# Optimization experiments

Hardware: AMD Instinct MI355X
Metric: run time of the kernel (lower is better)

The kernel has to match this reference:

```python
import jax, jax.numpy as jnp
import numpy as np

EMB = 768
HEADS = 12
HEAD_DIM = EMB // HEADS
SEQ = 4096
BATCH = 1


def setup_inputs() -> dict:
    key = jax.random.key(0)
    ks = jax.random.split(key, 9)
    s = 1.0 / np.sqrt(EMB)
    return {
        "x": jax.random.normal(ks[0], (BATCH, SEQ, EMB), dtype=jnp.float32),
        "wq": jax.random.normal(ks[1], (EMB, EMB), dtype=jnp.float32) * s,
        "bq": jax.random.normal(ks[2], (EMB,), dtype=jnp.float32) * s,
        "wk": jax.random.normal(ks[3], (EMB, EMB), dtype=jnp.float32) * s,
        "bk": jax.random.normal(ks[4], (EMB,), dtype=jnp.float32) * s,
        "wv": jax.random.normal(ks[5], (EMB, EMB), dtype=jnp.float32) * s,
        "bv": jax.random.normal(ks[6], (EMB,), dtype=jnp.float32) * s,
        "wo": jax.random.normal(ks[7], (EMB, EMB), dtype=jnp.float32) * s,
        "bo": jax.random.normal(ks[8], (EMB,), dtype=jnp.float32) * s,
    }


def reference(x, wq, bq, wk, bk, wv, bv, wo, bo):
    b, n, _ = x.shape
    # projections: [b, n, emb] -> [b, heads, n, head_dim]
    def split_heads(t):
        return t.reshape(b, n, HEADS, HEAD_DIM).transpose(0, 2, 1, 3)
    q = split_heads(x @ wq + bq)
    k = split_heads(x @ wk + bk)
    v = split_heads(x @ wv + bv)
    # full N x N scores (naive attention, as in the original)
    scores = jnp.einsum("bhqd,bhkd->bhqk", q, k)
    causal = jnp.triu(jnp.ones((n, n), dtype=bool), k=1)
    scores = jnp.where(causal, -jnp.inf, scores)
    weights = jax.nn.softmax(scores / np.sqrt(HEAD_DIM), axis=-1)
    # dropout with rate 0.0 is identity (eval mode)
    ctx = jnp.einsum("bhqk,bhkd->bhqd", weights, v)
    ctx = ctx.transpose(0, 2, 1, 3).reshape(b, n, EMB)
    return ctx @ wo + bo
```

## Files before the change

### kernel.cpp

```cpp
#include <hip/hip_runtime.h>
#include <stdint.h>

#define SEQ 4096
#define EMB 768
#define HEADS 12
#define HD 64

typedef __attribute__((ext_vector_type(8))) short short8;
typedef __attribute__((ext_vector_type(4))) short short4v;
typedef __attribute__((ext_vector_type(8))) __bf16 bf16x8;
typedef __attribute__((ext_vector_type(4))) __bf16 bf16x4;
typedef __attribute__((ext_vector_type(4))) float f32x4;

#define QSCALE 0.18033688011112043f

static __device__ __forceinline__ unsigned short f2bf(float f) {
    unsigned int u = __builtin_bit_cast(unsigned int, f);
    unsigned int r = 0x7fffu + ((u >> 16) & 1u);
    u += r;
    return (unsigned short)(u >> 16);
}

static __device__ __forceinline__ f32x4 mfma32(short8 a, short8 b, f32x4 c) {
    return __builtin_amdgcn_mfma_f32_16x16x32_bf16(
        __builtin_bit_cast(bf16x8, a), __builtin_bit_cast(bf16x8, b), c, 0, 0, 0);
}

static __device__ __forceinline__ f32x4 mfma16(short4v a, short4v b, f32x4 c) {
#if __has_builtin(__builtin_amdgcn_mfma_f32_16x16x16_bf16)
    return __builtin_amdgcn_mfma_f32_16x16x16_bf16(
        __builtin_bit_cast(bf16x4, a), __builtin_bit_cast(bf16x4, b), c, 0, 0, 0);
#else
    return __builtin_amdgcn_mfma_f32_16x16x16bf16_1k(a, b, c, 0, 0, 0);
#endif
}

static __device__ __forceinline__ short4v pack4bf(float a, float b, float c, float d) {
#if __has_builtin(__builtin_amdgcn_cvt_pk_bf16_f32)
    typedef __attribute__((ext_vector_type(2))) __bf16 bf16x2;
    bf16x2 lo = __builtin_amdgcn_cvt_pk_bf16_f32(a, b);
    bf16x2 hi = __builtin_amdgcn_cvt_pk_bf16_f32(c, d);
    uint2 u = {__builtin_bit_cast(unsigned int, lo), __builtin_bit_cast(unsigned int, hi)};
    return __builtin_bit_cast(short4v, u);
#else
    short4v p;
    p[0] = (short)f2bf(a); p[1] = (short)f2bf(b);
    p[2] = (short)f2bf(c); p[3] = (short)f2bf(d);
    return p;
#endif
}

static __device__ __forceinline__ void load_lds16(const void* g, void* l) {
    __builtin_amdgcn_global_load_lds(
        (const __attribute__((address_space(1))) unsigned int*)(uintptr_t)g,
        (__attribute__((address_space(3))) unsigned int*)(uintptr_t)l, 16, 0, 0);
}

static __device__ __forceinline__ int pid_coarse(int h, int i128, int ch) {
    int b = (i128 < 20) ? (i128 - 10)
                        : (i128 < 30 ? 10 + (i128 - 20) * 2 : 30 + (i128 - 30) * 3);
    return h * 36 + b + (ch - 1);
}

static __device__ __forceinline__ int pid_fine(int h, int i128, int ch) {
    int b = (i128 < 10) ? i128
          : (i128 < 20) ? 10 + (i128 - 10) * 3
          : (i128 < 30) ? 40 + (i128 - 20) * 5
                        : 90 + (i128 - 30) * 7;
    return h * 104 + b + (ch - 1);
}

static __device__ __forceinline__ void softmax_q(f32x4* st, float& m_i, float& l_i,
                                                 f32x4* O, short4v* pk) {
    float t0 = fmaxf(fmaxf(st[0][0], st[0][1]), fmaxf(st[0][2], st[0][3]));
    float t1 = fmaxf(fmaxf(st[1][0], st[1][1]), fmaxf(st[1][2], st[1][3]));
    float t2 = fmaxf(fmaxf(st[2][0], st[2][1]), fmaxf(st[2][2], st[2][3]));
    float t3 = fmaxf(fmaxf(st[3][0], st[3][1]), fmaxf(st[3][2], st[3][3]));
    float mx = fmaxf(fmaxf(t0, t1), fmaxf(t2, t3));
    if (__ballot(mx > m_i + 5.0f)) {
        mx = fmaxf(mx, __shfl_xor(mx, 16));
        mx = fmaxf(mx, __shfl_xor(mx, 32));
        const bool inc = mx > m_i;
        const float mn = inc ? mx : m_i;
        const float alpha = __builtin_amdgcn_exp2f(m_i - mn);
        m_i = mn;
        l_i *= alpha;
        for (int dt = 0; dt < 4; dt++)
            for (int r = 0; r < 4; r++) O[dt][r] *= alpha;
    }
    float rs = 0.f;
    for (int nt = 0; nt < 4; nt++) {
        float p0 = __builtin_amdgcn_exp2f(st[nt][0] - m_i);
        float p1 = __builtin_amdgcn_exp2f(st[nt][1] - m_i);
        float p2 = __builtin_amdgcn_exp2f(st[nt][2] - m_i);
        float p3 = __builtin_amdgcn_exp2f(st[nt][3] - m_i);
        rs += p0 + p1 + p2 + p3;
        pk[nt] = pack4bf(p0, p1, p2, p3);
    }
    l_i += rs;
}

__global__ __launch_bounds__(256) void convert_all(const float* __restrict__ x,
                                                   const float* __restrict__ wq,
                                                   const float* __restrict__ wk,
                                                   const float* __restrict__ wv,
                                                   const float* __restrict__ wo,
                                                   unsigned short* __restrict__ xb,
                                                   unsigned short* __restrict__ wqkvT,
                                                   unsigned short* __restrict__ woT) {
    __shared__ float Ls[64][65];
    const int bid = blockIdx.x;
    if (bid < 3072) {
        int i = bid * 256 + threadIdx.x;
        float4 v = ((const float4*)x)[i];
        ushort4 o = {f2bf(v.x), f2bf(v.y), f2bf(v.z), f2bf(v.w)};
        ((ushort4*)xb)[i] = o;
        return;
    }
    const int idx = bid - 3072;
    const int z = idx / 144;
    const int bx = (idx % 144) / 12, by = idx % 12;
    const float* W = (z == 0) ? wq : (z == 1) ? wk : (z == 2) ? wv : wo;
    unsigned short* dst = (z < 3) ? (wqkvT + (size_t)z * EMB * EMB) : woT;
    const int k0 = bx * 64, n0 = by * 64;
    const int r = threadIdx.x >> 2, c0 = (threadIdx.x & 3) * 16;
    for (int j = 0; j < 16; j += 4) {
        float4 v = *(const float4*)&W[(size_t)(k0 + r) * EMB + n0 + c0 + j];
        Ls[r][c0 + j] = v.x;
        Ls[r][c0 + j + 1] = v.y;
        Ls[r][c0 + j + 2] = v.z;
        Ls[r][c0 + j + 3] = v.w;
    }
    __syncthreads();
    unsigned short tmp[16];
    for (int j = 0; j < 16; j++) tmp[j] = f2bf(Ls[c0 + j][r]);
    *(uint4*)&dst[(size_t)(n0 + r) * EMB + k0 + c0] = *(uint4*)tmp;
    *(uint4*)&dst[(size_t)(n0 + r) * EMB + k0 + c0 + 8] = *(uint4*)(tmp + 8);
}

__global__ __launch_bounds__(256) void gemm_qkv(const unsigned short* __restrict__ A,
                                                const unsigned short* __restrict__ Bt,
                                                const float* __restrict__ b0p,
                                                const float* __restrict__ b1p,
                                                const float* __restrict__ b2p,
                                                unsigned short* __restrict__ QKb,
                                                unsigned short* __restrict__ Vtb) {
    __shared__ __align__(16) unsigned short SMEM[16384];
    const int tid = threadIdx.x;
    const int wave = tid >> 6, lane = tid & 63, quad = lane >> 4, l16 = lane & 15;
    const int m0 = blockIdx.x * 128, n0 = blockIdx.y * 128;
    const int wm = (wave >> 1) * 64, wn = (wave & 1) * 64;
    const int lrow = lane >> 2, lcol = (lane & 3) * 8;

    f32x4 acc[4][4] = {};

    for (int t = 0; t < 2; t++) {
        int row = wave * 32 + t * 16 + lrow;
        load_lds16(&A[(size_t)(m0 + row) * EMB + lcol], &SMEM[(wave * 2 + t) * 512]);
        load_lds16(&Bt[(size_t)(n0 + row) * EMB + lcol], &SMEM[4096 + (wave * 2 + t) * 512]);
    }
    int buf = 0;
    for (int k0 = 0; k0 < EMB; k0 += 32) {
        __syncthreads();
        if (k0 + 32 < EMB) {
            unsigned short* A_ = &SMEM[(buf ^ 1) * 8192];
            unsigned short* B_ = A_ + 4096;
            for (int t = 0; t < 2; t++) {
                int row = wave * 32 + t * 16 + lrow;
                load_lds16(&A[(size_t)(m0 + row) * EMB + k0 + 32 + lcol], &A_[(wave * 2 + t) * 512]);
                load_lds16(&Bt[(size_t)(n0 + row) * EMB + k0 + 32 + lcol], &B_[(wave * 2 + t) * 512]);
            }
        }
        const unsigned short* A_ = &SMEM[buf * 8192];
        const unsigned short* B_ = A_ + 4096;
        short8 a[4], b[4];
        for (int i = 0; i < 4; i++) a[i] = *(const short8*)&A_[(wm + i * 16 + l16) * 32 + quad * 8];
        for (int i = 0; i < 4; i++) b[i] = *(const short8*)&B_[(wn + i * 16 + l16) * 32 + quad * 8];
        for (int i = 0; i < 4; i++)
            for (int j = 0; j < 4; j++) acc[i][j] = mfma32(a[i], b[j], acc[i][j]);
        buf ^= 1;
    }

    const int z = n0 / EMB;
    if (z < 2) {
        const float* bias = z ? b1p : b0p;
        const float sc = z ? 1.0f : QSCALE;
        for (int i = 0; i < 4; i++)
            for (int j = 0; j < 4; j++) {
                int mbase = m0 + wm + i * 16 + quad * 4;
                int n = n0 + wn + j * 16 + l16;
                float bv = bias[n - z * EMB];
                for (int r = 0; r < 4; r++)
                    QKb[(size_t)(mbase + r) * 1536 + n] = f2bf((acc[i][j][r] + bv) * sc);
            }
    } else {
        const int nn = n0 + wn + l16 - 2 * EMB;
        for (int j = 0; j < 4; j++) {
            __syncthreads();
            const float bv = b2p[nn + j * 16];
            const int nloc = (wave & 1) * 16 + l16;
            for (int i = 0; i < 4; i++) {
                ushort4 pk;
                pk.x = f2bf(acc[i][j][0] + bv);
                pk.y = f2bf(acc[i][j][1] + bv);
                pk.z = f2bf(acc[i][j][2] + bv);
                pk.w = f2bf(acc[i][j][3] + bv);
                *(ushort4*)&SMEM[nloc * 136 + wm + i * 16 + quad * 4] = pk;
            }
            __syncthreads();
            const int nl = tid >> 3, c = tid & 7;
            const int ng = (nl >> 4) * 64 + j * 16 + (nl & 15) + n0 - 2 * EMB;
            const int hh = ng >> 6, dd = ng & 63;
            unsigned short* dst = &Vtb[(size_t)(hh * HD + dd) * SEQ + m0];
            *(uint4*)&dst[c * 8] = *(uint4*)&SMEM[nl * 136 + c * 8];
            *(uint4*)&dst[64 + c * 8] = *(uint4*)&SMEM[nl * 136 + 64 + c * 8];
        }
    }
}

__global__ __launch_bounds__(256) void gemm_out(const unsigned short* __restrict__ A,
                                                const unsigned short* __restrict__ Bt,
                                                const float* __restrict__ bias,
                                                float* __restrict__ outp) {
    __shared__ __align__(16) unsigned short SMEM[12288];
    const int tid = threadIdx.x;
    const int wave = tid >> 6, lane = tid & 63, quad = lane >> 4, l16 = lane & 15;
    const int m0 = blockIdx.x * 64, n0 = blockIdx.y * 128;
    const int wm = (wave >> 1) * 32, wn = (wave & 1) * 64;
    const int lrow = lane >> 2, lcol = (lane & 3) * 8;

    f32x4 acc[2][4] = {};

    load_lds16(&A[(size_t)(m0 + wave * 16 + lrow) * EMB + lcol], &SMEM[wave * 512]);
    for (int t = 0; t < 2; t++) {
        int row = wave * 32 + t * 16 + lrow;
        load_lds16(&Bt[(size_t)(n0 + row) * EMB + lcol], &SMEM[4096 + (wave * 2 + t) * 512]);
    }
    int buf = 0;
    for (int k0 = 0; k0 < EMB; k0 += 32) {
        __syncthreads();
        if (k0 + 32 < EMB) {
            unsigned short* A_ = &SMEM[(buf ^ 1) * 2048];
            unsigned short* B_ = &SMEM[4096 + (buf ^ 1) * 4096];
            load_lds16(&A[(size_t)(m0 + wave * 16 + lrow) * EMB + k0 + 32 + lcol], &A_[wave * 512]);
            for (int t = 0; t < 2; t++) {
                int row = wave * 32 + t * 16 + lrow;
                load_lds16(&Bt[(size_t)(n0 + row) * EMB + k0 + 32 + lcol], &B_[(wave * 2 + t) * 512]);
            }
        }
        const unsigned short* A_ = &SMEM[buf * 2048];
        const unsigned short* B_ = &SMEM[4096 + buf * 4096];
        short8 a[2], b[4];
        for (int i = 0; i < 2; i++) a[i] = *(const short8*)&A_[(wm + i * 16 + l16) * 32 + quad * 8];
        for (int j = 0; j < 4; j++) b[j] = *(const short8*)&B_[(wn + j * 16 + l16) * 32 + quad * 8];
        for (int i = 0; i < 2; i++)
            for (int j = 0; j < 4; j++) acc[i][j] = mfma32(a[i], b[j], acc[i][j]);
        buf ^= 1;
    }

    for (int i = 0; i < 2; i++)
        for (int j = 0; j < 4; j++) {
            int mbase = m0 + wm + i * 16 + quad * 4;
            int n = n0 + wn + j * 16 + l16;
            float bv = bias[n];
            for (int r = 0; r < 4; r++) outp[(size_t)(mbase + r) * EMB + n] = acc[i][j][r] + bv;
        }
}

template <bool FINE>
__global__ __launch_bounds__(256, 3) void attn_kernel(const unsigned short* __restrict__ QKb,
                                                      const unsigned short* __restrict__ Vtb,
                                                      unsigned short* __restrict__ ctxb,
                                                      unsigned short* __restrict__ Op,
                                                      float* __restrict__ mArr,
                                                      float* __restrict__ lArr) {
    __shared__ __align__(16) unsigned short Ks[64 * 64];
    __shared__ __align__(16) unsigned short Vs[2][64 * 64];

    const int bid = blockIdx.x;
    const int h = bid % HEADS;
    int i128, ch, nch;
    if (FINE) {
        const int r2 = 135 - bid / HEADS;
        if (r2 < 20) {
            i128 = r2 >> 1; ch = r2 & 1; nch = 2;
        } else if (r2 < 60) {
            int t = r2 - 20; i128 = 10 + (t >> 2); ch = t & 3; nch = 4;
        } else if (r2 < 120) {
            int t = r2 - 60; i128 = 20 + t / 6; ch = t % 6; nch = 6;
        } else {
            int t = r2 - 120; i128 = 30 + (t >> 3); ch = t & 7; nch = 8;
        }
    } else {
        const int r2 = 67 - bid / HEADS;
        if (r2 < 10) {
            i128 = r2; ch = 0; nch = 1;
        } else if (r2 < 30) {
            int t = r2 - 10; i128 = 10 + (t >> 1); ch = t & 1; nch = 2;
        } else if (r2 < 60) {
            int t = r2 - 30; i128 = 20 + t / 3; ch = t % 3; nch = 3;
        } else {
            int t = r2 - 60; i128 = 30 + (t >> 2); ch = t & 3; nch = 4;
        }
    }
    const int T = 2 * i128 + 2;
    const int kb = ch * T / nch;
    const int ke = (ch + 1) * T / nch - 1;
    const int qbase = i128 * 128;
    const int tid = threadIdx.x;
    const int wave = tid >> 6, lane = tid & 63, quad = lane >> 4, l16 = lane & 15;

    const unsigned short* Qg = QKb + (size_t)h * HD;
    const unsigned short* Kg = QKb + (size_t)(EMB + h * HD);
    const unsigned short* Vh = Vtb + (size_t)h * HD * SEQ;

    const int qa = qbase + wave * 32 + l16;
    const int qb = qa + 16;
    const short8 bQ0a = *(const short8*)&Qg[(size_t)qa * 1536 + quad * 8];
    const short8 bQ1a = *(const short8*)&Qg[(size_t)qa * 1536 + 32 + quad * 8];
    const short8 bQ0b = *(const short8*)&Qg[(size_t)qb * 1536 + quad * 8];
    const short8 bQ1b = *(const short8*)&Qg[(size_t)qb * 1536 + 32 + quad * 8];

    const int row = tid >> 2, t4 = tid & 3;
    const int swk = row & 7, swv = row & 15;

    f32x4 Oa[4] = {}, Ob[4] = {};
    float m_a = -3.0e38f, l_a = 0.f;
    float m_b = -3.0e38f, l_b = 0.f;

    uint4 kr0, kr1, vr0, vr1;
    {
        const int kb64 = kb * 64;
        const unsigned short* kp = &Kg[(size_t)(kb64 + row) * 1536];
        kr0 = *(const uint4*)&kp[(2 * t4) * 8];
        kr1 = *(const uint4*)&kp[(2 * t4 + 1) * 8];
        const unsigned short* vp = &Vh[(size_t)row * SEQ + kb64];
        vr0 = *(const uint4*)&vp[t4 * 16];
        vr1 = *(const uint4*)&vp[t4 * 16 + 8];
    }
    *(uint4*)&Ks[row * 64 + ((2 * t4) ^ swk) * 8] = kr0;
    *(uint4*)&Ks[row * 64 + ((2 * t4 + 1) ^ swk) * 8] = kr1;
    *(uint2*)&Vs[0][row * 64 + ((4 * t4) ^ swv) * 4] = ((const uint2*)&vr0)[0];
    *(uint2*)&Vs[0][row * 64 + ((4 * t4 + 1) ^ swv) * 4] = ((const uint2*)&vr0)[1];
    *(uint2*)&Vs[0][row * 64 + ((4 * t4 + 2) ^ swv) * 4] = ((const uint2*)&vr1)[0];
    *(uint2*)&Vs[0][row * 64 + ((4 * t4 + 3) ^ swv) * 4] = ((const uint2*)&vr1)[1];
    if (kb < ke) {
        const int nb = (kb + 1) * 64;
        const unsigned short* kp = &Kg[(size_t)(nb + row) * 1536];
        kr0 = *(const uint4*)&kp[(2 * t4) * 8];
        kr1 = *(const uint4*)&kp[(2 * t4 + 1) * 8];
        const unsigned short* vp = &Vh[(size_t)row * SEQ + nb];
        vr0 = *(const uint4*)&vp[t4 * 16];
        vr1 = *(const uint4*)&vp[t4 * 16 + 8];
    }
    __syncthreads();

    const int qw = qbase + wave * 32 + 31;
    const int swr = l16 & 7;

    f32x4 sa[4], sb[4];
    if (kb * 64 <= qw) {
        for (int nt = 0; nt < 4; nt++) {
            short8 aK0 = *(const short8*)&Ks[(nt * 16 + l16) * 64 + (quad ^ swr) * 8];
            short8 aK1 = *(const short8*)&Ks[(nt * 16 + l16) * 64 + ((quad + 4) ^ swr) * 8];
            f32x4 za = {};
            za = mfma32(aK0, bQ0a, za);
            za = mfma32(aK1, bQ1a, za);
            sa[nt] = za;
            f32x4 zb = {};
            zb = mfma32(aK0, bQ0b, zb);
            zb = mfma32(aK1, bQ1b, zb);
            sb[nt] = zb;
        }
        if (kb * 64 + 63 > qbase + wave * 32) {
            for (int nt = 0; nt < 4; nt++)
                for (int r = 0; r < 4; r++) {
                    const int kk = kb * 64 + nt * 16 + quad * 4 + r;
                    if (kk > qa) sa[nt][r] = -INFINITY;
                    if (kk > qb) sb[nt][r] = -INFINITY;
                }
        }
    }

    int p = 0;
    for (int kt = kb; kt <= ke; kt++) {
        __syncthreads();
        if (kt < ke) {
            *(uint4*)&Ks[row * 64 + ((2 * t4) ^ swk) * 8] = kr0;
            *(uint4*)&Ks[row * 64 + ((2 * t4 + 1) ^ swk) * 8] = kr1;
            *(uint2*)&Vs[p ^ 1][row * 64 + ((4 * t4) ^ swv) * 4] = ((const uint2*)&vr0)[0];
            *(uint2*)&Vs[p ^ 1][row * 64 + ((4 * t4 + 1) ^ swv) * 4] = ((const uint2*)&vr0)[1];
            *(uint2*)&Vs[p ^ 1][row * 64 + ((4 * t4 + 2) ^ swv) * 4] = ((const uint2*)&vr1)[0];
            *(uint2*)&Vs[p ^ 1][row * 64 + ((4 * t4 + 3) ^ swv) * 4] = ((const uint2*)&vr1)[1];
            if (kt + 1 < ke) {
                const int nb = (kt + 2) * 64;
                const unsigned short* kp = &Kg[(size_t)(nb + row) * 1536];
                kr0 = *(const uint4*)&kp[(2 * t4) * 8];
                kr1 = *(const uint4*)&kp[(2 * t4 + 1) * 8];
                const unsigned short* vp = &Vh[(size_t)row * SEQ + nb];
                vr0 = *(const uint4*)&vp[t4 * 16];
                vr1 = *(const uint4*)&vp[t4 * 16 + 8];
            }
        }
        __syncthreads();

        const int kbase = kt * 64;
        const bool cur = (kbase <= qw);

        short4v pka[4], pkb[4];
        if (cur) {
            softmax_q(sa, m_a, l_a, Oa, pka);
            softmax_q(sb, m_b, l_b, Ob, pkb);
        }

        const int kn = kbase + 64;
        if (kt < ke && kn <= qw) {
            for (int nt = 0; nt < 4; nt++) {
                short8 aK0 = *(const short8*)&Ks[(nt * 16 + l16) * 64 + (quad ^ swr) * 8];
                short8 aK1 = *(const short8*)&Ks[(nt * 16 + l16) * 64 + ((quad + 4) ^ swr) * 8];
                f32x4 za = {};
                za = mfma32(aK0, bQ0a, za);
                za = mfma32(aK1, bQ1a, za);
                sa[nt] = za;
                f32x4 zb = {};
                zb = mfma32(aK0, bQ0b, zb);
                zb = mfma32(aK1, bQ1b, zb);
                sb[nt] = zb;
            }
            if (kn + 63 > qbase + wave * 32) {
                for (int nt = 0; nt < 4; nt++)
                    for (int r = 0; r < 4; r++) {
                        const int kk = kn + nt * 16 + quad * 4 + r;
                        if (kk > qa) sa[nt][r] = -INFINITY;
                        if (kk > qb) sb[nt][r] = -INFINITY;
                    }
            }
        }

        if (cur) {
            for (int dt = 0; dt < 4; dt++)
                for (int nt = 0; nt < 4; nt++) {
                    short4v av =
                        *(const short4v*)&Vs[p][(dt * 16 + l16) * 64 + ((4 * nt + quad) ^ l16) * 4];
                    Oa[dt] = mfma16(av, pka[nt], Oa[dt]);
                    Ob[dt] = mfma16(av, pkb[nt], Ob[dt]);
                }
        }

        p ^= 1;
    }

    l_a += __shfl_xor(l_a, 16);
    l_a += __shfl_xor(l_a, 32);
    l_b += __shfl_xor(l_b, 16);
    l_b += __shfl_xor(l_b, 32);

    const int qla = wave * 32 + l16;
    const int qlb = qla + 16;
    if (!FINE && nch == 1) {
        const float ia = 1.f / l_a, ib = 1.f / l_b;
        for (int dt = 0; dt < 4; dt++) {
            ushort4 oa, ob;
            oa.x = f2bf(Oa[dt][0] * ia);
            oa.y = f2bf(Oa[dt][1] * ia);
            oa.z = f2bf(Oa[dt][2] * ia);
            oa.w = f2bf(Oa[dt][3] * ia);
            ob.x = f2bf(Ob[dt][0] * ib);
            ob.y = f2bf(Ob[dt][1] * ib);
            ob.z = f2bf(Ob[dt][2] * ib);
            ob.w = f2bf(Ob[dt][3] * ib);
            *(ushort4*)&ctxb[(size_t)qa * EMB + h * HD + dt * 16 + quad * 4] = oa;
            *(ushort4*)&ctxb[(size_t)qb * EMB + h * HD + dt * 16 + quad * 4] = ob;
        }
    } else {
        if (ch == 0) {
            for (int dt = 0; dt < 4; dt++) {
                ushort4 oa, ob;
                oa.x = f2bf(Oa[dt][0]);
                oa.y = f2bf(Oa[dt][1]);
                oa.z = f2bf(Oa[dt][2]);
                oa.w = f2bf(Oa[dt][3]);
                ob.x = f2bf(Ob[dt][0]);
                ob.y = f2bf(Ob[dt][1]);
                ob.z = f2bf(Ob[dt][2]);
                ob.w = f2bf(Ob[dt][3]);
                *(ushort4*)&ctxb[(size_t)qa * EMB + h * HD + dt * 16 + quad * 4] = oa;
                *(ushort4*)&ctxb[(size_t)qb * EMB + h * HD + dt * 16 + quad * 4] = ob;
            }
        } else {
            const int pid = FINE ? pid_fine(h, i128, ch) : pid_coarse(h, i128, ch);
            for (int dt = 0; dt < 4; dt++) {
                ushort4 oa, ob;
                oa.x = f2bf(Oa[dt][0]);
                oa.y = f2bf(Oa[dt][1]);
                oa.z = f2bf(Oa[dt][2]);
                oa.w = f2bf(Oa[dt][3]);
                ob.x = f2bf(Ob[dt][0]);
                ob.y = f2bf(Ob[dt][1]);
                ob.z = f2bf(Ob[dt][2]);
                ob.w = f2bf(Ob[dt][3]);
                *(ushort4*)&Op[(size_t)pid * 8192 + qla * 64 + dt * 16 + quad * 4] = oa;
                *(ushort4*)&Op[(size_t)pid * 8192 + qlb * 64 + dt * 16 + quad * 4] = ob;
            }
        }
        if (quad == 0) {
            const int MLS = FINE ? 8 : 4;
            const int mlb = ((h * 32 + i128) * MLS + ch) * 128;
            mArr[mlb + qla] = m_a;
            lArr[mlb + qla] = l_a;
            mArr[mlb + qlb] = m_b;
            lArr[mlb + qlb] = l_b;
        }
    }
}

template <bool FINE>
__global__ __launch_bounds__(256) void merge_kernel(const unsigned short* __restrict__ Op,
                                                    const float* __restrict__ mArr,
                                                    const float* __restrict__ lArr,
                                                    unsigned short* __restrict__ ctxb) {
    const int gid = blockIdx.x;
    const int h = gid % HEADS;
    const int i128 = FINE ? (gid / HEADS) : (10 + gid / HEADS);
    int nch;
    if (FINE)
        nch = (i128 < 10) ? 2 : (i128 < 20) ? 4 : (i128 < 30) ? 6 : 8;
    else
        nch = (i128 < 20) ? 2 : (i128 < 30) ? 3 : 4;
    const int MLS = FINE ? 8 : 4;
    const int q = threadIdx.x >> 1, d0 = (threadIdx.x & 1) * 32;
    const int mlbase = (h * 32 + i128) * MLS;

    float mc[8], lc[8];
    for (int c = 0; c < nch; c++) {
        mc[c] = mArr[(mlbase + c) * 128 + q];
        lc[c] = lArr[(mlbase + c) * 128 + q];
    }
    float M = mc[0];
    for (int c = 1; c < nch; c++) M = fmaxf(M, mc[c]);
    float w[8], L = 0.f;
    for (int c = 0; c < nch; c++) {
        w[c] = __builtin_amdgcn_exp2f(mc[c] - M);
        L += w[c] * lc[c];
    }
    const float inv = 1.f / L;
    for (int c = 0; c < nch; c++) w[c] *= inv;

    unsigned short* dst = &ctxb[(size_t)(i128 * 128 + q) * EMB + h * HD + d0];
    for (int jj = 0; jj < 32; jj += 8) {
        uint4 u0 = *(const uint4*)&dst[jj];
        float f[8];
        const unsigned short* p0 = (const unsigned short*)&u0;
        for (int t = 0; t < 8; t++)
            f[t] = w[0] * __builtin_bit_cast(float, (unsigned int)p0[t] << 16);
        for (int c = 1; c < nch; c++) {
            const int pid = FINE ? pid_fine(h, i128, c) : pid_coarse(h, i128, c);
            uint4 u = *(const uint4*)&Op[(size_t)pid * 8192 + q * 64 + d0 + jj];
            const unsigned short* p = (const unsigned short*)&u;
            for (int t = 0; t < 8; t++)
                f[t] += w[c] * __builtin_bit_cast(float, (unsigned int)p[t] << 16);
        }
        unsigned short o[8];
        for (int t = 0; t < 8; t++) o[t] = f2bf(f[t]);
        *(uint4*)&dst[jj] = *(uint4*)o;
    }
}

extern "C" void kernel_launch(void* const* d_in, const int* in_sizes, int n_in,
                              void* d_out, int out_size, void* d_ws, size_t ws_size,
                              hipStream_t stream) {
    const float* x = (const float*)d_in[0];
    const float* wq = (const float*)d_in[1];
    const float* bq = (const float*)d_in[2];
    const float* wk = (const float*)d_in[3];
    const float* bk = (const float*)d_in[4];
    const float* wv = (const float*)d_in[5];
    const float* bv = (const float*)d_in[6];
    const float* wo = (const float*)d_in[7];
    const float* bo = (const float*)d_in[8];

    unsigned short* ws = (unsigned short*)d_ws;
    unsigned short* xb = ws;
    unsigned short* wqkvT = xb + SEQ * EMB;
    unsigned short* woT = wqkvT + 3 * EMB * EMB;
    unsigned short* QKb = woT + EMB * EMB;
    unsigned short* Vtb = QKb + (size_t)SEQ * 1536;
    unsigned short* ctxb = Vtb + HEADS * SEQ * HD;

    convert_all<<<dim3(3072 + 576), 256, 0, stream>>>(x, wq, wk, wv, wo, xb, wqkvT, woT);
    gemm_qkv<<<dim3(SEQ / 128, 3 * EMB / 128), 256, 0, stream>>>(
        xb, wqkvT, bq, bk, bv, QKb, Vtb);

    const bool fine = ws_size >= (size_t)29884416 * 2;
    if (fine) {
        unsigned short* OpF = ws + 18087936u;
        float* mF = (float*)(ws + 28311552u);
        float* lF = mF + 393216;
        attn_kernel<true><<<dim3(12 * 136), 256, 0, stream>>>(QKb, Vtb, ctxb, OpF, mF, lF);
        merge_kernel<true><<<dim3(12 * 32), 256, 0, stream>>>(OpF, mF, lF, ctxb);
    } else {
        unsigned short* Op = xb;
        float* mArr = (float*)(ws + 3538944);
        float* lArr = mArr + 196608;
        attn_kernel<false><<<dim3(12 * 68), 256, 0, stream>>>(QKb, Vtb, ctxb, Op, mArr, lArr);
        merge_kernel<false><<<dim3(264), 256, 0, stream>>>(Op, mArr, lArr, ctxb);
    }
    gemm_out<<<dim3(SEQ / 64, EMB / 128), 256, 0, stream>>>(ctxb, woT, bo, (float*)d_out);
}
```

Before: 191.1 us.

## Load K tiles directly into registers, drop K shared buffer and a barrier

```diff
diff --git a/kernel.cpp b/kernel.cpp
--- a/kernel.cpp
+++ b/kernel.cpp
@@ -268,13 +268,12 @@
 }
 
 template <bool FINE>
-__global__ __launch_bounds__(256, 3) void attn_kernel(const unsigned short* __restrict__ QKb,
+__global__ __launch_bounds__(256, 4) void attn_kernel(const unsigned short* __restrict__ QKb,
                                                       const unsigned short* __restrict__ Vtb,
                                                       unsigned short* __restrict__ ctxb,
                                                       unsigned short* __restrict__ Op,
                                                       float* __restrict__ mArr,
                                                       float* __restrict__ lArr) {
-    __shared__ __align__(16) unsigned short Ks[64 * 64];
     __shared__ __align__(16) unsigned short Vs[2][64 * 64];
 
     const int bid = blockIdx.x;
@@ -322,54 +321,50 @@
     const short8 bQ1b = *(const short8*)&Qg[(size_t)qb * 1536 + 32 + quad * 8];
 
     const int row = tid >> 2, t4 = tid & 3;
-    const int swk = row & 7, swv = row & 15;
+    const int swv = row & 15;
 
     f32x4 Oa[4] = {}, Ob[4] = {};
     float m_a = -3.0e38f, l_a = 0.f;
     float m_b = -3.0e38f, l_b = 0.f;
 
-    uint4 kr0, kr1, vr0, vr1;
+    uint4 vr0, vr1;
     {
-        const int kb64 = kb * 64;
-        const unsigned short* kp = &Kg[(size_t)(kb64 + row) * 1536];
-        kr0 = *(const uint4*)&kp[(2 * t4) * 8];
-        kr1 = *(const uint4*)&kp[(2 * t4 + 1) * 8];
-        const unsigned short* vp = &Vh[(size_t)row * SEQ + kb64];
+        const unsigned short* vp = &Vh[(size_t)row * SEQ + kb * 64];
         vr0 = *(const uint4*)&vp[t4 * 16];
         vr1 = *(const uint4*)&vp[t4 * 16 + 8];
     }
-    *(uint4*)&Ks[row * 64 + ((2 * t4) ^ swk) * 8] = kr0;
-    *(uint4*)&Ks[row * 64 + ((2 * t4 + 1) ^ swk) * 8] = kr1;
     *(uint2*)&Vs[0][row * 64 + ((4 * t4) ^ swv) * 4] = ((const uint2*)&vr0)[0];
     *(uint2*)&Vs[0][row * 64 + ((4 * t4 + 1) ^ swv) * 4] = ((const uint2*)&vr0)[1];
     *(uint2*)&Vs[0][row * 64 + ((4 * t4 + 2) ^ swv) * 4] = ((const uint2*)&vr1)[0];
     *(uint2*)&Vs[0][row * 64 + ((4 * t4 + 3) ^ swv) * 4] = ((const uint2*)&vr1)[1];
     if (kb < ke) {
-        const int nb = (kb + 1) * 64;
-        const unsigned short* kp = &Kg[(size_t)(nb + row) * 1536];
-        kr0 = *(const uint4*)&kp[(2 * t4) * 8];
-        kr1 = *(const uint4*)&kp[(2 * t4 + 1) * 8];
-        const unsigned short* vp = &Vh[(size_t)row * SEQ + nb];
+        const unsigned short* vp = &Vh[(size_t)row * SEQ + (kb + 1) * 64];
         vr0 = *(const uint4*)&vp[t4 * 16];
         vr1 = *(const uint4*)&vp[t4 * 16 + 8];
     }
+
+    const int qw = qbase + wave * 32 + 31;
+
+    short8 k0[4], k1[4];
+    if (kb * 64 <= qw) {
+        for (int nt = 0; nt < 4; nt++) {
+            const unsigned short* kp = &Kg[(size_t)(kb * 64 + nt * 16 + l16) * 1536 + quad * 8];
+            k0[nt] = *(const short8*)kp;
+            k1[nt] = *(const short8*)&kp[32];
+        }
+    }
     __syncthreads();
-
-    const int qw = qbase + wave * 32 + 31;
-    const int swr = l16 & 7;
 
     f32x4 sa[4], sb[4];
     if (kb * 64 <= qw) {
         for (int nt = 0; nt < 4; nt++) {
-            short8 aK0 = *(const short8*)&Ks[(nt * 16 + l16) * 64 + (quad ^ swr) * 8];
-            short8 aK1 = *(const short8*)&Ks[(nt * 16 + l16) * 64 + ((quad + 4) ^ swr) * 8];
             f32x4 za = {};
-            za = mfma32(aK0, bQ0a, za);
-            za = mfma32(aK1, bQ1a, za);
+            za = mfma32(k0[nt], bQ0a, za);
+            za = mfma32(k1[nt], bQ1a, za);
             sa[nt] = za;
             f32x4 zb = {};
-            zb = mfma32(aK0, bQ0b, zb);
-            zb = mfma32(aK1, bQ1b, zb);
+            zb = mfma32(k0[nt], bQ0b, zb);
+            zb = mfma32(k1[nt], bQ1b, zb);
             sb[nt] = zb;
         }
         if (kb * 64 + 63 > qbase + wave * 32) {
@@ -381,28 +376,28 @@
                 }
         }
     }
+    if (kb + 1 <= ke && (kb + 1) * 64 <= qw) {
+        for (int nt = 0; nt < 4; nt++) {
+            const unsigned short* kp =
+                &Kg[(size_t)((kb + 1) * 64 + nt * 16 + l16) * 1536 + quad * 8];
+            k0[nt] = *(const short8*)kp;
+            k1[nt] = *(const short8*)&kp[32];
+        }
+    }
 
     int p = 0;
     for (int kt = kb; kt <= ke; kt++) {
-        __syncthreads();
         if (kt < ke) {
-            *(uint4*)&Ks[row * 64 + ((2 * t4) ^ swk) * 8] = kr0;
-            *(uint4*)&Ks[row * 64 + ((2 * t4 + 1) ^ swk) * 8] = kr1;
             *(uint2*)&Vs[p ^ 1][row * 64 + ((4 * t4) ^ swv) * 4] = ((const uint2*)&vr0)[0];
             *(uint2*)&Vs[p ^ 1][row * 64 + ((4 * t4 + 1) ^ swv) * 4] = ((const uint2*)&vr0)[1];
             *(uint2*)&Vs[p ^ 1][row * 64 + ((4 * t4 + 2) ^ swv) * 4] = ((const uint2*)&vr1)[0];
             *(uint2*)&Vs[p ^ 1][row * 64 + ((4 * t4 + 3) ^ swv) * 4] = ((const uint2*)&vr1)[1];
             if (kt + 1 < ke) {
-                const int nb = (kt + 2) * 64;
-                const unsigned short* kp = &Kg[(size_t)(nb + row) * 1536];
-                kr0 = *(const uint4*)&kp[(2 * t4) * 8];
-                kr1 = *(const uint4*)&kp[(2 * t4 + 1) * 8];
-                const unsigned short* vp = &Vh[(size_t)row * SEQ + nb];
+                const unsigned short* vp = &Vh[(size_t)row * SEQ + (kt + 2) * 64];
                 vr0 = *(const uint4*)&vp[t4 * 16];
                 vr1 = *(const uint4*)&vp[t4 * 16 + 8];
             }
         }
-        __syncthreads();
 
         const int kbase = kt * 64;
         const bool cur = (kbase <= qw);
@@ -416,15 +411,13 @@
         const int kn = kbase + 64;
         if (kt < ke && kn <= qw) {
             for (int nt = 0; nt < 4; nt++) {
-                short8 aK0 = *(const short8*)&Ks[(nt * 16 + l16) * 64 + (quad ^ swr) * 8];
-                short8 aK1 = *(const short8*)&Ks[(nt * 16 + l16) * 64 + ((quad + 4) ^ swr) * 8];
                 f32x4 za = {};
-                za = mfma32(aK0, bQ0a, za);
-                za = mfma32(aK1, bQ1a, za);
+                za = mfma32(k0[nt], bQ0a, za);
+                za = mfma32(k1[nt], bQ1a, za);
                 sa[nt] = za;
                 f32x4 zb = {};
-                zb = mfma32(aK0, bQ0b, zb);
-                zb = mfma32(aK1, bQ1b, zb);
+                zb = mfma32(k0[nt], bQ0b, zb);
+                zb = mfma32(k1[nt], bQ1b, zb);
                 sb[nt] = zb;
             }
             if (kn + 63 > qbase + wave * 32) {
@@ -434,6 +427,14 @@
                         if (kk > qa) sa[nt][r] = -INFINITY;
                         if (kk > qb) sb[nt][r] = -INFINITY;
                     }
+            }
+            if (kt + 2 <= ke && (kt + 2) * 64 <= qw) {
+                for (int nt = 0; nt < 4; nt++) {
+                    const unsigned short* kp =
+                        &Kg[(size_t)((kt + 2) * 64 + nt * 16 + l16) * 1536 + quad * 8];
+                    k0[nt] = *(const short8*)kp;
+                    k1[nt] = *(const short8*)&kp[32];
+                }
             }
         }
 
@@ -447,6 +448,7 @@
                 }
         }
 
+        __syncthreads();
         p ^= 1;
     }
 
```

Result: slower. 387.5 us (+102.8%).
